# Kernel tuning notes

Measured on AMD Instinct MI355X. Metric: run time of the kernel, lower is better.

Reference implementation:

```python
import jax, jax.numpy as jnp
import numpy as np

N_NODES = 100000


def _sage_conv(x, edge_index, W_n, W_s, b):
    # edge_index: [2, E] with row0 = src, row1 = dst (messages flow src -> dst)
    src, dst = edge_index[0], edge_index[1]
    msgs = x[src]                                   # [E, F] gather
    summed = jax.ops.segment_sum(msgs, dst, num_segments=N_NODES)   # [N, F]
    deg = jax.ops.segment_sum(jnp.ones((edge_index.shape[1],), x.dtype), dst,
                              num_segments=N_NODES)                 # [N]
    mean = summed / jnp.maximum(deg, 1.0)[:, None]  # mean aggregation
    return mean @ W_n + x @ W_s + b


def setup_inputs() -> dict:
    key = jax.random.key(0)
    ks = jax.random.split(key, 8)
    in_dim, hid_dim, out_dim = 64, 64, 32
    n_edges = 1600000
    x = jax.random.normal(ks[0], (N_NODES, in_dim), dtype=jnp.float32)
    edge_index = jax.random.randint(ks[1], (2, n_edges), 0, N_NODES, dtype=jnp.int64)
    s1 = 1.0 / np.sqrt(in_dim)
    s2 = 1.0 / np.sqrt(hid_dim)
    W1_n = jax.random.uniform(ks[2], (in_dim, hid_dim), jnp.float32, -s1, s1)
    W1_s = jax.random.uniform(ks[3], (in_dim, hid_dim), jnp.float32, -s1, s1)
    b1 = jnp.zeros((hid_dim,), jnp.float32)
    W2_n = jax.random.uniform(ks[4], (hid_dim, out_dim), jnp.float32, -s2, s2)
    W2_s = jax.random.uniform(ks[5], (hid_dim, out_dim), jnp.float32, -s2, s2)
    b2 = jnp.zeros((out_dim,), jnp.float32)
    return {"x": x, "edge_index": edge_index, "W1_n": W1_n, "W1_s": W1_s,
            "b1": b1, "W2_n": W2_n, "W2_s": W2_s, "b2": b2}


def reference(x, edge_index, W1_n, W1_s, b1, W2_n, W2_s, b2):
    h = _sage_conv(x, edge_index, W1_n, W1_s, b1)
    h = jax.nn.relu(h)
    # dropout(p=0.5) is identity in eval mode
    out = _sage_conv(h, edge_index, W2_n, W2_s, b2)
    return out
```

## Files before the change

kernel.cpp:

```cpp
#include <hip/hip_runtime.h>
#include <hip/hip_bf16.h>

#define N_NODES 100000
#define NB 784
#define NPAD 100352
#define BSH 7
#define BMASK 127
#define CAP 4096

typedef float v2f __attribute__((ext_vector_type(2)));

__device__ inline void fma4(float a, const float4& w, float4& c) {
  c.x = fmaf(a, w.x, c.x);
  c.y = fmaf(a, w.y, c.y);
  c.z = fmaf(a, w.z, c.z);
  c.w = fmaf(a, w.w, c.w);
}
__device__ inline unsigned short f2bf(float f) {
  unsigned u = __float_as_uint(f);
  u += 0x7fffu + ((u >> 16) & 1u);
  return (unsigned short)(u >> 16);
}
__device__ inline unsigned pack2bf(float a, float b) {
  return (unsigned)f2bf(a) | ((unsigned)f2bf(b) << 16);
}
__device__ inline float bf2f(unsigned short u) {
  return __uint_as_float((unsigned)u << 16);
}
__device__ inline unsigned packfp8x4(float a, float b, float c, float d) {
  int pk = __builtin_amdgcn_cvt_pk_fp8_f32(a, b, 0, false);
  pk = __builtin_amdgcn_cvt_pk_fp8_f32(c, d, pk, true);
  return (unsigned)pk;
}
__device__ inline float4 relu_mix(uint2 m, uint2 s) {
  float4 v;
  v.x = fmaxf(__uint_as_float(m.x << 16) + __uint_as_float(s.x << 16), 0.f);
  v.y = fmaxf(__uint_as_float(m.x & 0xffff0000u) +
                  __uint_as_float(s.x & 0xffff0000u), 0.f);
  v.z = fmaxf(__uint_as_float(m.y << 16) + __uint_as_float(s.y << 16), 0.f);
  v.w = fmaxf(__uint_as_float(m.y & 0xffff0000u) +
                  __uint_as_float(s.y & 0xffff0000u), 0.f);
  return v;
}

#define EPB 4096
#define GB1 1563

__global__ __launch_bounds__(256) void fusedA_k(
    const int* __restrict__ src, const int* __restrict__ dst,
    unsigned* __restrict__ bcur, unsigned* __restrict__ ep,
    const float* __restrict__ x, const float* __restrict__ W1n,
    const float* __restrict__ W1s, const float* __restrict__ b1,
    unsigned* __restrict__ xnb8, unsigned short* __restrict__ xsb,
    int E, int NSB, int M) {
  __shared__ __align__(16) float smem[8192];
  const int tid = threadIdx.x;

  if ((int)blockIdx.x < NSB) {
    unsigned* lh = (unsigned*)smem;
    unsigned* lbase = lh + NB;
    for (int i = tid; i < NB; i += 256) lh[i] = 0;
    __syncthreads();
    const int base = blockIdx.x * EPB;
    unsigned short rank[16];
    unsigned short bb[16];
#pragma unroll
    for (int it = 0; it < 16; ++it) {
      int e = base + it * 256 + tid;
      if (e < E) {
        unsigned b = ((unsigned)dst[e]) >> BSH;
        bb[it] = (unsigned short)b;
        rank[it] = (unsigned short)atomicAdd(&lh[b], 1u);
      }
    }
    __syncthreads();
    for (int i = tid; i < NB; i += 256)
      lbase[i] = lh[i] ? atomicAdd(&bcur[i], lh[i]) : 0u;
    __syncthreads();
#pragma unroll
    for (int it = 0; it < 16; ++it) {
      int e = base + it * 256 + tid;
      if (e < E) {
        unsigned b = bb[it];
        ep[(size_t)b * CAP + lbase[b] + rank[it]] =
            (((unsigned)src[e]) << BSH) | (((unsigned)dst[e]) & BMASK);
      }
    }
    return;
  }

  float* Wn = smem;
  float* Ws = smem + 4096;
  const int row0 = ((int)blockIdx.x - NSB) * 64;

  for (int i = tid; i < 1024; i += 256) {
    ((float4*)Wn)[i] = ((const float4*)W1n)[i];
    ((float4*)Ws)[i] = ((const float4*)W1s)[i];
  }

  const int tx = tid & 15;
  const int ty = tid >> 4;
  const int arow = ty * 4;

  const float* xr[4];
#pragma unroll
  for (int r = 0; r < 4; ++r) {
    long long gr = row0 + arow + r;
    if (gr >= M) gr = M - 1;
    xr[r] = x + gr * 64;
  }

  float4 an[4], as[4];
#pragma unroll
  for (int r = 0; r < 4; ++r) {
    an[r] = make_float4(0.f, 0.f, 0.f, 0.f);
    as[r] = make_float4(0.f, 0.f, 0.f, 0.f);
  }
  __syncthreads();

#pragma unroll 2
  for (int k4 = 0; k4 < 16; ++k4) {
    float4 a[4];
#pragma unroll
    for (int r = 0; r < 4; ++r) a[r] = *(const float4*)(xr[r] + 4 * k4);
    float4 wn0 = *(const float4*)&Wn[(4 * k4 + 0) * 64 + 4 * tx];
    float4 wn1 = *(const float4*)&Wn[(4 * k4 + 1) * 64 + 4 * tx];
    float4 wn2 = *(const float4*)&Wn[(4 * k4 + 2) * 64 + 4 * tx];
    float4 wn3 = *(const float4*)&Wn[(4 * k4 + 3) * 64 + 4 * tx];
    float4 ws0 = *(const float4*)&Ws[(4 * k4 + 0) * 64 + 4 * tx];
    float4 ws1 = *(const float4*)&Ws[(4 * k4 + 1) * 64 + 4 * tx];
    float4 ws2 = *(const float4*)&Ws[(4 * k4 + 2) * 64 + 4 * tx];
    float4 ws3 = *(const float4*)&Ws[(4 * k4 + 3) * 64 + 4 * tx];
#pragma unroll
    for (int r = 0; r < 4; ++r) {
      fma4(a[r].x, wn0, an[r]);
      fma4(a[r].y, wn1, an[r]);
      fma4(a[r].z, wn2, an[r]);
      fma4(a[r].w, wn3, an[r]);
      fma4(a[r].x, ws0, as[r]);
      fma4(a[r].y, ws1, as[r]);
      fma4(a[r].z, ws2, as[r]);
      fma4(a[r].w, ws3, as[r]);
    }
  }

  const float4 bv = *(const float4*)&b1[4 * tx];
#pragma unroll
  for (int r = 0; r < 4; ++r) {
    int row = row0 + arow + r;
    if (row < M) {
      ushort4 ps;
      ps.x = f2bf(as[r].x + bv.x);
      ps.y = f2bf(as[r].y + bv.y);
      ps.z = f2bf(as[r].z + bv.z);
      ps.w = f2bf(as[r].w + bv.w);
      *(ushort4*)&xsb[(long long)row * 64 + 4 * tx] = ps;
      xnb8[(size_t)row * 16 + tx] =
          packfp8x4(an[r].x, an[r].y, an[r].z, an[r].w);
    }
  }
}

__global__ __launch_bounds__(256) void bsort_k(const unsigned* __restrict__ ep,
                                               const unsigned* __restrict__ bcur,
                                               int* __restrict__ ssrc,
                                               uint2* __restrict__ rows2) {
  __shared__ unsigned cnt[128];
  __shared__ unsigned sc[128];
  const int tid = threadIdx.x;
  const int b = blockIdx.x;
  const unsigned cntb = bcur[b];
  const unsigned beg = (unsigned)(b * CAP);
  if (tid < 128) cnt[tid] = 0;
  __syncthreads();
  for (unsigned j = tid; j < cntb; j += 256)
    atomicAdd(&cnt[ep[(size_t)beg + j] & BMASK], 1u);
  __syncthreads();
  unsigned v = (tid < 128) ? cnt[tid] : 0u;
  if (tid < 128) sc[tid] = v;
  __syncthreads();
  for (int off = 1; off < 128; off <<= 1) {
    unsigned t = (tid < 128 && tid >= off) ? sc[tid - off] : 0u;
    __syncthreads();
    if (tid < 128) sc[tid] += t;
    __syncthreads();
  }
  if (tid < 128) {
    unsigned ex = sc[tid] - v;
    rows2[b * 128 + tid] = make_uint2(beg + ex, beg + ex + v);
    cnt[tid] = ex;
  }
  __syncthreads();
  for (unsigned j = tid; j < cntb; j += 256) {
    unsigned p = ep[(size_t)beg + j];
    unsigned r = atomicAdd(&cnt[p & BMASK], 1u);
    ssrc[(size_t)beg + r] = (int)(p >> BSH);
  }
}

#define MSTRIDE 36

__global__ __launch_bounds__(256) void fgg_k(
    const uint4* __restrict__ valb4, const int* __restrict__ ssrc,
    const uint2* __restrict__ rows2, const unsigned short* __restrict__ xsb,
    const float* __restrict__ W2n, const float* __restrict__ W2s,
    const float* __restrict__ b2, unsigned* __restrict__ hnb8,
    float* __restrict__ hs, int M) {
  __shared__ float Wn[64 * 32];
  __shared__ float Ws[64 * 32];
  __shared__ unsigned mlds[64 * MSTRIDE];
  const int tid = threadIdx.x;
  const int node0 = blockIdx.x * 64;

  for (int i = tid; i < 512; i += 256) {
    ((float4*)Wn)[i] = ((const float4*)W2n)[i];
    ((float4*)Ws)[i] = ((const float4*)W2s)[i];
  }

  constexpr int P = 4;
  const int lrow = tid / P;
  const int node = node0 + lrow;
  const int p = tid & 3;
  const uint2 be = rows2[node];
  const unsigned beg = be.x, end = be.y;

  float acc[16];
#pragma unroll
  for (int q = 0; q < 16; ++q) acc[q] = 0.f;

  unsigned j = beg;
  for (; j + 8 <= end; j += 8) {
    int sn[8];
#pragma unroll
    for (int i = 0; i < 8; ++i) sn[i] = ssrc[j + i];
    uint4 u[8];
#pragma unroll
    for (int i = 0; i < 8; ++i) u[i] = valb4[(size_t)sn[i] * P + p];
#pragma unroll
    for (int i = 0; i < 8; ++i) {
      v2f f0 = __builtin_amdgcn_cvt_pk_f32_fp8((int)u[i].x, false);
      v2f f1 = __builtin_amdgcn_cvt_pk_f32_fp8((int)u[i].x, true);
      v2f f2 = __builtin_amdgcn_cvt_pk_f32_fp8((int)u[i].y, false);
      v2f f3 = __builtin_amdgcn_cvt_pk_f32_fp8((int)u[i].y, true);
      v2f f4 = __builtin_amdgcn_cvt_pk_f32_fp8((int)u[i].z, false);
      v2f f5 = __builtin_amdgcn_cvt_pk_f32_fp8((int)u[i].z, true);
      v2f f6 = __builtin_amdgcn_cvt_pk_f32_fp8((int)u[i].w, false);
      v2f f7 = __builtin_amdgcn_cvt_pk_f32_fp8((int)u[i].w, true);
      acc[0] += f0[0];  acc[1] += f0[1];
      acc[2] += f1[0];  acc[3] += f1[1];
      acc[4] += f2[0];  acc[5] += f2[1];
      acc[6] += f3[0];  acc[7] += f3[1];
      acc[8] += f4[0];  acc[9] += f4[1];
      acc[10] += f5[0]; acc[11] += f5[1];
      acc[12] += f6[0]; acc[13] += f6[1];
      acc[14] += f7[0]; acc[15] += f7[1];
    }
  }
  if (j < end) {
    const unsigned last = end - 1;
    int sn[8];
#pragma unroll
    for (int i = 0; i < 8; ++i) {
      unsigned jj = j + i;
      sn[i] = ssrc[jj < last ? jj : last];
    }
    uint4 u[8];
#pragma unroll
    for (int i = 0; i < 8; ++i) u[i] = valb4[(size_t)sn[i] * P + p];
#pragma unroll
    for (int i = 0; i < 8; ++i) {
      float w = ((j + i) < end) ? 1.f : 0.f;
      v2f f0 = __builtin_amdgcn_cvt_pk_f32_fp8((int)u[i].x, false);
      v2f f1 = __builtin_amdgcn_cvt_pk_f32_fp8((int)u[i].x, true);
      v2f f2 = __builtin_amdgcn_cvt_pk_f32_fp8((int)u[i].y, false);
      v2f f3 = __builtin_amdgcn_cvt_pk_f32_fp8((int)u[i].y, true);
      v2f f4 = __builtin_amdgcn_cvt_pk_f32_fp8((int)u[i].z, false);
      v2f f5 = __builtin_amdgcn_cvt_pk_f32_fp8((int)u[i].z, true);
      v2f f6 = __builtin_amdgcn_cvt_pk_f32_fp8((int)u[i].w, false);
      v2f f7 = __builtin_amdgcn_cvt_pk_f32_fp8((int)u[i].w, true);
      acc[0] = fmaf(w, f0[0], acc[0]);   acc[1] = fmaf(w, f0[1], acc[1]);
      acc[2] = fmaf(w, f1[0], acc[2]);   acc[3] = fmaf(w, f1[1], acc[3]);
      acc[4] = fmaf(w, f2[0], acc[4]);   acc[5] = fmaf(w, f2[1], acc[5]);
      acc[6] = fmaf(w, f3[0], acc[6]);   acc[7] = fmaf(w, f3[1], acc[7]);
      acc[8] = fmaf(w, f4[0], acc[8]);   acc[9] = fmaf(w, f4[1], acc[9]);
      acc[10] = fmaf(w, f5[0], acc[10]); acc[11] = fmaf(w, f5[1], acc[11]);
      acc[12] = fmaf(w, f6[0], acc[12]); acc[13] = fmaf(w, f6[1], acc[13]);
      acc[14] = fmaf(w, f7[0], acc[14]); acc[15] = fmaf(w, f7[1], acc[15]);
    }
  }

  const unsigned dg = end - beg;
  const float inv = dg ? 1.f / (float)dg : 0.f;
  uint4 pk0, pk1;
  pk0.x = pack2bf(acc[0] * inv, acc[1] * inv);
  pk0.y = pack2bf(acc[2] * inv, acc[3] * inv);
  pk0.z = pack2bf(acc[4] * inv, acc[5] * inv);
  pk0.w = pack2bf(acc[6] * inv, acc[7] * inv);
  pk1.x = pack2bf(acc[8] * inv, acc[9] * inv);
  pk1.y = pack2bf(acc[10] * inv, acc[11] * inv);
  pk1.z = pack2bf(acc[12] * inv, acc[13] * inv);
  pk1.w = pack2bf(acc[14] * inv, acc[15] * inv);
  *(uint4*)&mlds[lrow * MSTRIDE + p * 8] = pk0;
  *(uint4*)&mlds[lrow * MSTRIDE + p * 8 + 4] = pk1;
  __syncthreads();

  const int tx = tid & 7;
  const int ty = tid >> 3;
  const int arow = ty * 2;

  const uint2* mp[2];
  const uint2* sp[2];
#pragma unroll
  for (int r = 0; r < 2; ++r) {
    long long gr = node0 + arow + r;
    if (gr >= M) gr = M - 1;
    mp[r] = (const uint2*)&mlds[(arow + r) * MSTRIDE];
    sp[r] = (const uint2*)(xsb + gr * 64);
  }

  float4 an[2], as[2];
#pragma unroll
  for (int r = 0; r < 2; ++r) {
    an[r] = make_float4(0.f, 0.f, 0.f, 0.f);
    as[r] = make_float4(0.f, 0.f, 0.f, 0.f);
  }

#pragma unroll 2
  for (int k4 = 0; k4 < 16; ++k4) {
    float4 a[2];
#pragma unroll
    for (int r = 0; r < 2; ++r) a[r] = relu_mix(mp[r][k4], sp[r][k4]);
    float4 wn0 = *(const float4*)&Wn[(4 * k4 + 0) * 32 + 4 * tx];
    float4 wn1 = *(const float4*)&Wn[(4 * k4 + 1) * 32 + 4 * tx];
    float4 wn2 = *(const float4*)&Wn[(4 * k4 + 2) * 32 + 4 * tx];
    float4 wn3 = *(const float4*)&Wn[(4 * k4 + 3) * 32 + 4 * tx];
    float4 ws0 = *(const float4*)&Ws[(4 * k4 + 0) * 32 + 4 * tx];
    float4 ws1 = *(const float4*)&Ws[(4 * k4 + 1) * 32 + 4 * tx];
    float4 ws2 = *(const float4*)&Ws[(4 * k4 + 2) * 32 + 4 * tx];
    float4 ws3 = *(const float4*)&Ws[(4 * k4 + 3) * 32 + 4 * tx];
#pragma unroll
    for (int r = 0; r < 2; ++r) {
      fma4(a[r].x, wn0, an[r]);
      fma4(a[r].y, wn1, an[r]);
      fma4(a[r].z, wn2, an[r]);
      fma4(a[r].w, wn3, an[r]);
      fma4(a[r].x, ws0, as[r]);
      fma4(a[r].y, ws1, as[r]);
      fma4(a[r].z, ws2, as[r]);
      fma4(a[r].w, ws3, as[r]);
    }
  }

  const float4 bv = *(const float4*)&b2[4 * tx];
#pragma unroll
  for (int r = 0; r < 2; ++r) {
    int row = node0 + arow + r;
    if (row < M) {
      float4 o;
      o.x = as[r].x + bv.x;
      o.y = as[r].y + bv.y;
      o.z = as[r].z + bv.z;
      o.w = as[r].w + bv.w;
      *(float4*)&hs[(long long)row * 32 + 4 * tx] = o;
      hnb8[(size_t)row * 8 + tx] =
          packfp8x4(an[r].x, an[r].y, an[r].z, an[r].w);
    }
  }
}

__global__ __launch_bounds__(256) void gather2_k(
    const uint4* __restrict__ valb4, const int* __restrict__ ssrc,
    const uint2* __restrict__ rows2, const float* __restrict__ base,
    float* __restrict__ out, int N) {
  constexpr int P = 2;
  const int node = blockIdx.x * 128 + threadIdx.x / P;
  const int p = threadIdx.x & 1;
  if (node >= N) return;
  const uint2 be = rows2[node];
  const unsigned beg = be.x, end = be.y;

  float acc[16];
#pragma unroll
  for (int q = 0; q < 16; ++q) acc[q] = 0.f;

  unsigned j = beg;
  for (; j + 8 <= end; j += 8) {
    int sn[8];
#pragma unroll
    for (int i = 0; i < 8; ++i) sn[i] = ssrc[j + i];
    uint4 u[8];
#pragma unroll
    for (int i = 0; i < 8; ++i) u[i] = valb4[(size_t)sn[i] * P + p];
#pragma unroll
    for (int i = 0; i < 8; ++i) {
      v2f f0 = __builtin_amdgcn_cvt_pk_f32_fp8((int)u[i].x, false);
      v2f f1 = __builtin_amdgcn_cvt_pk_f32_fp8((int)u[i].x, true);
      v2f f2 = __builtin_amdgcn_cvt_pk_f32_fp8((int)u[i].y, false);
      v2f f3 = __builtin_amdgcn_cvt_pk_f32_fp8((int)u[i].y, true);
      v2f f4 = __builtin_amdgcn_cvt_pk_f32_fp8((int)u[i].z, false);
      v2f f5 = __builtin_amdgcn_cvt_pk_f32_fp8((int)u[i].z, true);
      v2f f6 = __builtin_amdgcn_cvt_pk_f32_fp8((int)u[i].w, false);
      v2f f7 = __builtin_amdgcn_cvt_pk_f32_fp8((int)u[i].w, true);
      acc[0] += f0[0];  acc[1] += f0[1];
      acc[2] += f1[0];  acc[3] += f1[1];
      acc[4] += f2[0];  acc[5] += f2[1];
      acc[6] += f3[0];  acc[7] += f3[1];
      acc[8] += f4[0];  acc[9] += f4[1];
      acc[10] += f5[0]; acc[11] += f5[1];
      acc[12] += f6[0]; acc[13] += f6[1];
      acc[14] += f7[0]; acc[15] += f7[1];
    }
  }
  if (j < end) {
    const unsigned last = end - 1;
    int sn[8];
#pragma unroll
    for (int i = 0; i < 8; ++i) {
      unsigned jj = j + i;
      sn[i] = ssrc[jj < last ? jj : last];
    }
    uint4 u[8];
#pragma unroll
    for (int i = 0; i < 8; ++i) u[i] = valb4[(size_t)sn[i] * P + p];
#pragma unroll
    for (int i = 0; i < 8; ++i) {
      float w = ((j + i) < end) ? 1.f : 0.f;
      v2f f0 = __builtin_amdgcn_cvt_pk_f32_fp8((int)u[i].x, false);
      v2f f1 = __builtin_amdgcn_cvt_pk_f32_fp8((int)u[i].x, true);
      v2f f2 = __builtin_amdgcn_cvt_pk_f32_fp8((int)u[i].y, false);
      v2f f3 = __builtin_amdgcn_cvt_pk_f32_fp8((int)u[i].y, true);
      v2f f4 = __builtin_amdgcn_cvt_pk_f32_fp8((int)u[i].z, false);
      v2f f5 = __builtin_amdgcn_cvt_pk_f32_fp8((int)u[i].z, true);
      v2f f6 = __builtin_amdgcn_cvt_pk_f32_fp8((int)u[i].w, false);
      v2f f7 = __builtin_amdgcn_cvt_pk_f32_fp8((int)u[i].w, true);
      acc[0] = fmaf(w, f0[0], acc[0]);   acc[1] = fmaf(w, f0[1], acc[1]);
      acc[2] = fmaf(w, f1[0], acc[2]);   acc[3] = fmaf(w, f1[1], acc[3]);
      acc[4] = fmaf(w, f2[0], acc[4]);   acc[5] = fmaf(w, f2[1], acc[5]);
      acc[6] = fmaf(w, f3[0], acc[6]);   acc[7] = fmaf(w, f3[1], acc[7]);
      acc[8] = fmaf(w, f4[0], acc[8]);   acc[9] = fmaf(w, f4[1], acc[9]);
      acc[10] = fmaf(w, f5[0], acc[10]); acc[11] = fmaf(w, f5[1], acc[11]);
      acc[12] = fmaf(w, f6[0], acc[12]); acc[13] = fmaf(w, f6[1], acc[13]);
      acc[14] = fmaf(w, f7[0], acc[14]); acc[15] = fmaf(w, f7[1], acc[15]);
    }
  }

  const unsigned dg = end - beg;
  const float inv = dg ? 1.f / (float)dg : 0.f;
  const size_t o = (size_t)node * 32 + 16 * p;
#pragma unroll
  for (int q4 = 0; q4 < 4; ++q4) {
    float4 bv = *(const float4*)&base[o + 4 * q4];
    float4 ov;
    ov.x = acc[4 * q4 + 0] * inv + bv.x;
    ov.y = acc[4 * q4 + 1] * inv + bv.y;
    ov.z = acc[4 * q4 + 2] * inv + bv.z;
    ov.w = acc[4 * q4 + 3] * inv + bv.w;
    *(float4*)&out[o + 4 * q4] = ov;
  }
}

extern "C" void kernel_launch(void* const* d_in, const int* in_sizes, int n_in,
                              void* d_out, int out_size, void* d_ws,
                              size_t ws_size, hipStream_t stream) {
  const float* x   = (const float*)d_in[0];
  const int*   ei  = (const int*)d_in[1];
  const float* W1n = (const float*)d_in[2];
  const float* W1s = (const float*)d_in[3];
  const float* b1  = (const float*)d_in[4];
  const float* W2n = (const float*)d_in[5];
  const float* W2s = (const float*)d_in[6];
  const float* b2  = (const float*)d_in[7];
  float* out = (float*)d_out;

  const int E = in_sizes[1] / 2;
  const int M = N_NODES;
  const int* src = ei;
  const int* dst = ei + E;
  const int NSB = (E + EPB - 1) / EPB;

  char* wsb = (char*)d_ws;
  unsigned*       ep    = (unsigned*)(wsb);
  int*            ssrc  = (int*)(wsb + 12845056);
  uint2*          rows2 = (uint2*)(wsb + 25690112);
  unsigned*       bcur  = (unsigned*)(wsb + 26492928);
  unsigned*       xnb8  = (unsigned*)(wsb + 26496064);
  unsigned short* xsb   = (unsigned short*)(wsb + 32896064);
  float*          hs    = (float*)(wsb + 45696064);
  unsigned*       hnb8  = (unsigned*)(wsb);

  hipMemsetAsync(bcur, 0, NB * 4, stream);
  fusedA_k<<<NSB + GB1, 256, 0, stream>>>(src, dst, bcur, ep, x, W1n, W1s, b1,
                                          xnb8, xsb, E, NSB, M);
  bsort_k<<<NB, 256, 0, stream>>>(ep, bcur, ssrc, rows2);
  fgg_k<<<GB1, 256, 0, stream>>>((const uint4*)xnb8, ssrc, rows2, xsb, W2n,
                                 W2s, b2, hnb8, hs, M);
  gather2_k<<<(M + 127) / 128, 256, 0, stream>>>((const uint4*)hnb8, ssrc,
                                                 rows2, hs, out, M);
}
```

Measured before the change: 198.8 us.

## Fuse edge bucketing into layer-1 GEMM and bucket sort into layer-1 gather

Every layer-1 GEMM block now loads the weights, and the first NSB of them also scatter a 2048-edge chunk into dst buckets before doing their GEMM tile. The separate bucket-sort kernel is merged into the first gather+GEMM kernel: each block sorts one 128-node bucket, keeps the sorted source ids in LDS when they fit, and then aggregates and multiplies two 64-node halves. The intent is to remove a kernel launch and its round trip through global memory, and to reuse the sorted indices from LDS. In exchange the fused kernel runs fewer, heavier blocks (784 instead of 1563) and uses more LDS, which may lower occupancy. hnb8 is moved to its own workspace region because it can no longer alias ep.

```diff
diff --git a/kernel.cpp b/kernel.cpp
--- a/kernel.cpp
+++ b/kernel.cpp
@@ -7,6 +7,8 @@
 #define BSH 7
 #define BMASK 127
 #define CAP 4096
+#define LCAP 3584
+#define MSTRIDE 36
 
 typedef float v2f __attribute__((ext_vector_type(2)));
 
@@ -23,9 +25,6 @@
 }
 __device__ inline unsigned pack2bf(float a, float b) {
   return (unsigned)f2bf(a) | ((unsigned)f2bf(b) << 16);
-}
-__device__ inline float bf2f(unsigned short u) {
-  return __uint_as_float((unsigned)u << 16);
 }
 __device__ inline unsigned packfp8x4(float a, float b, float c, float d) {
   int pk = __builtin_amdgcn_cvt_pk_fp8_f32(a, b, 0, false);
@@ -43,10 +42,11 @@
   return v;
 }
 
-#define EPB 4096
+#define EPB 2048
+#define EPT 8
 #define GB1 1563
 
-__global__ __launch_bounds__(256) void fusedA_k(
+__global__ __launch_bounds__(256, 5) void fusedA_k(
     const int* __restrict__ src, const int* __restrict__ dst,
     unsigned* __restrict__ bcur, unsigned* __restrict__ ep,
     const float* __restrict__ x, const float* __restrict__ W1n,
@@ -54,23 +54,32 @@
     unsigned* __restrict__ xnb8, unsigned short* __restrict__ xsb,
     int E, int NSB, int M) {
   __shared__ __align__(16) float smem[8192];
+  float* Wn = smem;
+  float* Ws = smem + 4096;
+  unsigned* lh = (unsigned*)Ws;
+  unsigned* lbase = lh + NB;
   const int tid = threadIdx.x;
-
-  if ((int)blockIdx.x < NSB) {
-    unsigned* lh = (unsigned*)smem;
-    unsigned* lbase = lh + NB;
+  const int bid = blockIdx.x;
+
+  for (int i = tid; i < 1024; i += 256)
+    ((float4*)Wn)[i] = ((const float4*)W1n)[i];
+
+  if (bid < NSB) {
     for (int i = tid; i < NB; i += 256) lh[i] = 0;
     __syncthreads();
-    const int base = blockIdx.x * EPB;
-    unsigned short rank[16];
-    unsigned short bb[16];
-#pragma unroll
-    for (int it = 0; it < 16; ++it) {
-      int e = base + it * 256 + tid;
+    const int ebase = bid * EPB;
+    int es[EPT], ed[EPT];
+    unsigned short rk[EPT], bb[EPT];
+#pragma unroll
+    for (int it = 0; it < EPT; ++it) {
+      int e = ebase + it * 256 + tid;
       if (e < E) {
-        unsigned b = ((unsigned)dst[e]) >> BSH;
-        bb[it] = (unsigned short)b;
-        rank[it] = (unsigned short)atomicAdd(&lh[b], 1u);
+        int d = dst[e];
+        es[it] = src[e];
+        ed[it] = d;
+        unsigned bkt = ((unsigned)d) >> BSH;
+        bb[it] = (unsigned short)bkt;
+        rk[it] = (unsigned short)atomicAdd(&lh[bkt], 1u);
       }
     }
     __syncthreads();
@@ -78,26 +87,21 @@
       lbase[i] = lh[i] ? atomicAdd(&bcur[i], lh[i]) : 0u;
     __syncthreads();
 #pragma unroll
-    for (int it = 0; it < 16; ++it) {
-      int e = base + it * 256 + tid;
+    for (int it = 0; it < EPT; ++it) {
+      int e = ebase + it * 256 + tid;
       if (e < E) {
-        unsigned b = bb[it];
-        ep[(size_t)b * CAP + lbase[b] + rank[it]] =
-            (((unsigned)src[e]) << BSH) | (((unsigned)dst[e]) & BMASK);
-      }
-    }
-    return;
-  }
-
-  float* Wn = smem;
-  float* Ws = smem + 4096;
-  const int row0 = ((int)blockIdx.x - NSB) * 64;
-
-  for (int i = tid; i < 1024; i += 256) {
-    ((float4*)Wn)[i] = ((const float4*)W1n)[i];
+        unsigned bkt = bb[it];
+        ep[(size_t)bkt * CAP + lbase[bkt] + rk[it]] =
+            (((unsigned)es[it]) << BSH) | (((unsigned)ed[it]) & BMASK);
+      }
+    }
+    __syncthreads();
+  }
+
+  for (int i = tid; i < 1024; i += 256)
     ((float4*)Ws)[i] = ((const float4*)W1s)[i];
-  }
-
+
+  const int row0 = bid * 64;
   const int tx = tid & 15;
   const int ty = tid >> 4;
   const int arow = ty * 4;
@@ -161,18 +165,31 @@
   }
 }
 
-__global__ __launch_bounds__(256) void bsort_k(const unsigned* __restrict__ ep,
-                                               const unsigned* __restrict__ bcur,
-                                               int* __restrict__ ssrc,
-                                               uint2* __restrict__ rows2) {
+__global__ __launch_bounds__(256, 4) void fggs_k(
+    const uint4* __restrict__ valb4, const unsigned* __restrict__ ep,
+    const unsigned* __restrict__ bcur, int* __restrict__ ssrc,
+    uint2* __restrict__ rows2, const unsigned short* __restrict__ xsb,
+    const float* __restrict__ W2n, const float* __restrict__ W2s,
+    const float* __restrict__ b2, unsigned* __restrict__ hnb8,
+    float* __restrict__ hs, int M) {
+  __shared__ float Wn[64 * 32];
+  __shared__ float Ws[64 * 32];
+  __shared__ unsigned ssrc_l[LCAP];
+  __shared__ unsigned mlds[64 * MSTRIDE];
   __shared__ unsigned cnt[128];
   __shared__ unsigned sc[128];
   const int tid = threadIdx.x;
   const int b = blockIdx.x;
   const unsigned cntb = bcur[b];
   const unsigned beg = (unsigned)(b * CAP);
+
+  for (int i = tid; i < 512; i += 256) {
+    ((float4*)Wn)[i] = ((const float4*)W2n)[i];
+    ((float4*)Ws)[i] = ((const float4*)W2s)[i];
+  }
   if (tid < 128) cnt[tid] = 0;
   __syncthreads();
+
   for (unsigned j = tid; j < cntb; j += 256)
     atomicAdd(&cnt[ep[(size_t)beg + j] & BMASK], 1u);
   __syncthreads();
@@ -188,39 +205,188 @@
   if (tid < 128) {
     unsigned ex = sc[tid] - v;
     rows2[b * 128 + tid] = make_uint2(beg + ex, beg + ex + v);
-    cnt[tid] = ex;
-  }
+    cnt[tid] = ex | (v << 16);
+  }
+  __syncthreads();
+  const int ln = tid >> 2;
+  const int p4 = tid & 3;
+  const unsigned cpk0 = cnt[ln];
+  const unsigned cpk1 = cnt[64 + ln];
   __syncthreads();
   for (unsigned j = tid; j < cntb; j += 256) {
-    unsigned p = ep[(size_t)beg + j];
-    unsigned r = atomicAdd(&cnt[p & BMASK], 1u);
-    ssrc[(size_t)beg + r] = (int)(p >> BSH);
-  }
-}
-
-#define MSTRIDE 36
-
-__global__ __launch_bounds__(256) void fgg_k(
+    unsigned pv = ep[(size_t)beg + j];
+    unsigned r = atomicAdd(&cnt[pv & BMASK], 1u) & 0xffffu;
+    unsigned s = pv >> BSH;
+    ssrc[(size_t)beg + r] = (int)s;
+    if (r < LCAP) ssrc_l[r] = s;
+  }
+  __syncthreads();
+
+  const unsigned* sl = (cntb <= (unsigned)LCAP)
+                           ? (const unsigned*)ssrc_l
+                           : (const unsigned*)ssrc + beg;
+
+#pragma unroll
+  for (int pp = 0; pp < 2; ++pp) {
+    const unsigned cpk = pp ? cpk1 : cpk0;
+    const unsigned lbeg = cpk & 0xffffu;
+    const unsigned dg = cpk >> 16;
+    const unsigned lend = lbeg + dg;
+
+    float acc[16];
+#pragma unroll
+    for (int q = 0; q < 16; ++q) acc[q] = 0.f;
+
+    unsigned j = lbeg;
+    for (; j + 8 <= lend; j += 8) {
+      unsigned sn[8];
+#pragma unroll
+      for (int i = 0; i < 8; ++i) sn[i] = sl[j + i];
+      uint4 u[8];
+#pragma unroll
+      for (int i = 0; i < 8; ++i) u[i] = valb4[(size_t)sn[i] * 4 + p4];
+#pragma unroll
+      for (int i = 0; i < 8; ++i) {
+        v2f f0 = __builtin_amdgcn_cvt_pk_f32_fp8((int)u[i].x, false);
+        v2f f1 = __builtin_amdgcn_cvt_pk_f32_fp8((int)u[i].x, true);
+        v2f f2 = __builtin_amdgcn_cvt_pk_f32_fp8((int)u[i].y, false);
+        v2f f3 = __builtin_amdgcn_cvt_pk_f32_fp8((int)u[i].y, true);
+        v2f f4 = __builtin_amdgcn_cvt_pk_f32_fp8((int)u[i].z, false);
+        v2f f5 = __builtin_amdgcn_cvt_pk_f32_fp8((int)u[i].z, true);
+        v2f f6 = __builtin_amdgcn_cvt_pk_f32_fp8((int)u[i].w, false);
+        v2f f7 = __builtin_amdgcn_cvt_pk_f32_fp8((int)u[i].w, true);
+        acc[0] += f0[0];  acc[1] += f0[1];
+        acc[2] += f1[0];  acc[3] += f1[1];
+        acc[4] += f2[0];  acc[5] += f2[1];
+        acc[6] += f3[0];  acc[7] += f3[1];
+        acc[8] += f4[0];  acc[9] += f4[1];
+        acc[10] += f5[0]; acc[11] += f5[1];
+        acc[12] += f6[0]; acc[13] += f6[1];
+        acc[14] += f7[0]; acc[15] += f7[1];
+      }
+    }
+    if (j < lend) {
+      const unsigned last = lend - 1;
+      unsigned sn[8];
+#pragma unroll
+      for (int i = 0; i < 8; ++i) {
+        unsigned jj = j + i;
+        sn[i] = sl[jj < last ? jj : last];
+      }
+      uint4 u[8];
+#pragma unroll
+      for (int i = 0; i < 8; ++i) u[i] = valb4[(size_t)sn[i] * 4 + p4];
+#pragma unroll
+      for (int i = 0; i < 8; ++i) {
+        float w = ((j + i) < lend) ? 1.f : 0.f;
+        v2f f0 = __builtin_amdgcn_cvt_pk_f32_fp8((int)u[i].x, false);
+        v2f f1 = __builtin_amdgcn_cvt_pk_f32_fp8((int)u[i].x, true);
+        v2f f2 = __builtin_amdgcn_cvt_pk_f32_fp8((int)u[i].y, false);
+        v2f f3 = __builtin_amdgcn_cvt_pk_f32_fp8((int)u[i].y, true);
+        v2f f4 = __builtin_amdgcn_cvt_pk_f32_fp8((int)u[i].z, false);
+        v2f f5 = __builtin_amdgcn_cvt_pk_f32_fp8((int)u[i].z, true);
+        v2f f6 = __builtin_amdgcn_cvt_pk_f32_fp8((int)u[i].w, false);
+        v2f f7 = __builtin_amdgcn_cvt_pk_f32_fp8((int)u[i].w, true);
+        acc[0] = fmaf(w, f0[0], acc[0]);   acc[1] = fmaf(w, f0[1], acc[1]);
+        acc[2] = fmaf(w, f1[0], acc[2]);   acc[3] = fmaf(w, f1[1], acc[3]);
+        acc[4] = fmaf(w, f2[0], acc[4]);   acc[5] = fmaf(w, f2[1], acc[5]);
+        acc[6] = fmaf(w, f3[0], acc[6]);   acc[7] = fmaf(w, f3[1], acc[7]);
+        acc[8] = fmaf(w, f4[0], acc[8]);   acc[9] = fmaf(w, f4[1], acc[9]);
+        acc[10] = fmaf(w, f5[0], acc[10]); acc[11] = fmaf(w, f5[1], acc[11]);
+        acc[12] = fmaf(w, f6[0], acc[12]); acc[13] = fmaf(w, f6[1], acc[13]);
+        acc[14] = fmaf(w, f7[0], acc[14]); acc[15] = fmaf(w, f7[1], acc[15]);
+      }
+    }
+
+    const float inv = dg ? 1.f / (float)dg : 0.f;
+    uint4 pk0, pk1;
+    pk0.x = pack2bf(acc[0] * inv, acc[1] * inv);
+    pk0.y = pack2bf(acc[2] * inv, acc[3] * inv);
+    pk0.z = pack2bf(acc[4] * inv, acc[5] * inv);
+    pk0.w = pack2bf(acc[6] * inv, acc[7] * inv);
+    pk1.x = pack2bf(acc[8] * inv, acc[9] * inv);
+    pk1.y = pack2bf(acc[10] * inv, acc[11] * inv);
+    pk1.z = pack2bf(acc[12] * inv, acc[13] * inv);
+    pk1.w = pack2bf(acc[14] * inv, acc[15] * inv);
+    *(uint4*)&mlds[ln * MSTRIDE + p4 * 8] = pk0;
+    *(uint4*)&mlds[ln * MSTRIDE + p4 * 8 + 4] = pk1;
+    __syncthreads();
+
+    const int tx = tid & 7;
+    const int ty = tid >> 3;
+    const int arow = ty * 2;
+    const int node0p = b * 128 + pp * 64;
+
+    const uint2* mp[2];
+    const uint2* sp[2];
+#pragma unroll
+    for (int r = 0; r < 2; ++r) {
+      long long gr = node0p + arow + r;
+      if (gr >= M) gr = M - 1;
+      mp[r] = (const uint2*)&mlds[(arow + r) * MSTRIDE];
+      sp[r] = (const uint2*)(xsb + gr * 64);
+    }
+
+    float4 an[2], as[2];
+#pragma unroll
+    for (int r = 0; r < 2; ++r) {
+      an[r] = make_float4(0.f, 0.f, 0.f, 0.f);
+      as[r] = make_float4(0.f, 0.f, 0.f, 0.f);
+    }
+
+#pragma unroll 2
+    for (int k4 = 0; k4 < 16; ++k4) {
+      float4 a[2];
+#pragma unroll
+      for (int r = 0; r < 2; ++r) a[r] = relu_mix(mp[r][k4], sp[r][k4]);
+      float4 wn0 = *(const float4*)&Wn[(4 * k4 + 0) * 32 + 4 * tx];
+      float4 wn1 = *(const float4*)&Wn[(4 * k4 + 1) * 32 + 4 * tx];
+      float4 wn2 = *(const float4*)&Wn[(4 * k4 + 2) * 32 + 4 * tx];
+      float4 wn3 = *(const float4*)&Wn[(4 * k4 + 3) * 32 + 4 * tx];
+      float4 ws0 = *(const float4*)&Ws[(4 * k4 + 0) * 32 + 4 * tx];
+      float4 ws1 = *(const float4*)&Ws[(4 * k4 + 1) * 32 + 4 * tx];
+      float4 ws2 = *(const float4*)&Ws[(4 * k4 + 2) * 32 + 4 * tx];
+      float4 ws3 = *(const float4*)&Ws[(4 * k4 + 3) * 32 + 4 * tx];
+#pragma unroll
+      for (int r = 0; r < 2; ++r) {
+        fma4(a[r].x, wn0, an[r]);
+        fma4(a[r].y, wn1, an[r]);
+        fma4(a[r].z, wn2, an[r]);
+        fma4(a[r].w, wn3, an[r]);
+        fma4(a[r].x, ws0, as[r]);
+        fma4(a[r].y, ws1, as[r]);
+        fma4(a[r].z, ws2, as[r]);
+        fma4(a[r].w, ws3, as[r]);
+      }
+    }
+
+    const float4 bvv = *(const float4*)&b2[4 * tx];
+#pragma unroll
+    for (int r = 0; r < 2; ++r) {
+      int row = node0p + arow + r;
+      if (row < M) {
+        float4 o;
+        o.x = as[r].x + bvv.x;
+        o.y = as[r].y + bvv.y;
+        o.z = as[r].z + bvv.z;
+        o.w = as[r].w + bvv.w;
+        *(float4*)&hs[(long long)row * 32 + 4 * tx] = o;
+        hnb8[(size_t)row * 8 + tx] =
+            packfp8x4(an[r].x, an[r].y, an[r].z, an[r].w);
+      }
+    }
+    __syncthreads();
+  }
+}
+
+__global__ __launch_bounds__(256) void gather2_k(
     const uint4* __restrict__ valb4, const int* __restrict__ ssrc,
-    const uint2* __restrict__ rows2, const unsigned short* __restrict__ xsb,
-    const float* __restrict__ W2n, const float* __restrict__ W2s,
-    const float* __restrict__ b2, unsigned* __restrict__ hnb8,
-    float* __restrict__ hs, int M) {
-  __shared__ float Wn[64 * 32];
-  __shared__ float Ws[64 * 32];
-  __shared__ unsigned mlds[64 * MSTRIDE];
-  const int tid = threadIdx.x;
-  const int node0 = blockIdx.x * 64;
-
-  for (int i = tid; i < 512; i += 256) {
-    ((float4*)Wn)[i] = ((const float4*)W2n)[i];
-    ((float4*)Ws)[i] = ((const float4*)W2s)[i];
-  }
-
-  constexpr int P = 4;
-  const int lrow = tid / P;
-  const int node = node0 + lrow;
-  const int p = tid & 3;
+    const uint2* __restrict__ rows2, const float* __restrict__ base,
+    float* __restrict__ out, int N) {
+  constexpr int P = 2;
+  const int node = blockIdx.x * 128 + threadIdx.x / P;
+  const int p = threadIdx.x & 1;
+  if (node >= N) return;
   const uint2 be = rows2[node];
   const unsigned beg = be.x, end = be.y;
 
@@ -291,161 +457,6 @@
 
   const unsigned dg = end - beg;
   const float inv = dg ? 1.f / (float)dg : 0.f;
-  uint4 pk0, pk1;
-  pk0.x = pack2bf(acc[0] * inv, acc[1] * inv);
-  pk0.y = pack2bf(acc[2] * inv, acc[3] * inv);
-  pk0.z = pack2bf(acc[4] * inv, acc[5] * inv);
-  pk0.w = pack2bf(acc[6] * inv, acc[7] * inv);
-  pk1.x = pack2bf(acc[8] * inv, acc[9] * inv);
-  pk1.y = pack2bf(acc[10] * inv, acc[11] * inv);
-  pk1.z = pack2bf(acc[12] * inv, acc[13] * inv);
-  pk1.w = pack2bf(acc[14] * inv, acc[15] * inv);
-  *(uint4*)&mlds[lrow * MSTRIDE + p * 8] = pk0;
-  *(uint4*)&mlds[lrow * MSTRIDE + p * 8 + 4] = pk1;
-  __syncthreads();
-
-  const int tx = tid & 7;
-  const int ty = tid >> 3;
-  const int arow = ty * 2;
-
-  const uint2* mp[2];
-  const uint2* sp[2];
-#pragma unroll
-  for (int r = 0; r < 2; ++r) {
-    long long gr = node0 + arow + r;
-    if (gr >= M) gr = M - 1;
-    mp[r] = (const uint2*)&mlds[(arow + r) * MSTRIDE];
-    sp[r] = (const uint2*)(xsb + gr * 64);
-  }
-
-  float4 an[2], as[2];
-#pragma unroll
-  for (int r = 0; r < 2; ++r) {
-    an[r] = make_float4(0.f, 0.f, 0.f, 0.f);
-    as[r] = make_float4(0.f, 0.f, 0.f, 0.f);
-  }
-
-#pragma unroll 2
-  for (int k4 = 0; k4 < 16; ++k4) {
-    float4 a[2];
-#pragma unroll
-    for (int r = 0; r < 2; ++r) a[r] = relu_mix(mp[r][k4], sp[r][k4]);
-    float4 wn0 = *(const float4*)&Wn[(4 * k4 + 0) * 32 + 4 * tx];
-    float4 wn1 = *(const float4*)&Wn[(4 * k4 + 1) * 32 + 4 * tx];
-    float4 wn2 = *(const float4*)&Wn[(4 * k4 + 2) * 32 + 4 * tx];
-    float4 wn3 = *(const float4*)&Wn[(4 * k4 + 3) * 32 + 4 * tx];
-    float4 ws0 = *(const float4*)&Ws[(4 * k4 + 0) * 32 + 4 * tx];
-    float4 ws1 = *(const float4*)&Ws[(4 * k4 + 1) * 32 + 4 * tx];
-    float4 ws2 = *(const float4*)&Ws[(4 * k4 + 2) * 32 + 4 * tx];
-    float4 ws3 = *(const float4*)&Ws[(4 * k4 + 3) * 32 + 4 * tx];
-#pragma unroll
-    for (int r = 0; r < 2; ++r) {
-      fma4(a[r].x, wn0, an[r]);
-      fma4(a[r].y, wn1, an[r]);
-      fma4(a[r].z, wn2, an[r]);
-      fma4(a[r].w, wn3, an[r]);
-      fma4(a[r].x, ws0, as[r]);
-      fma4(a[r].y, ws1, as[r]);
-      fma4(a[r].z, ws2, as[r]);
-      fma4(a[r].w, ws3, as[r]);
-    }
-  }
-
-  const float4 bv = *(const float4*)&b2[4 * tx];
-#pragma unroll
-  for (int r = 0; r < 2; ++r) {
-    int row = node0 + arow + r;
-    if (row < M) {
-      float4 o;
-      o.x = as[r].x + bv.x;
-      o.y = as[r].y + bv.y;
-      o.z = as[r].z + bv.z;
-      o.w = as[r].w + bv.w;
-      *(float4*)&hs[(long long)row * 32 + 4 * tx] = o;
-      hnb8[(size_t)row * 8 + tx] =
-          packfp8x4(an[r].x, an[r].y, an[r].z, an[r].w);
-    }
-  }
-}
-
-__global__ __launch_bounds__(256) void gather2_k(
-    const uint4* __restrict__ valb4, const int* __restrict__ ssrc,
-    const uint2* __restrict__ rows2, const float* __restrict__ base,
-    float* __restrict__ out, int N) {
-  constexpr int P = 2;
-  const int node = blockIdx.x * 128 + threadIdx.x / P;
-  const int p = threadIdx.x & 1;
-  if (node >= N) return;
-  const uint2 be = rows2[node];
-  const unsigned beg = be.x, end = be.y;
-
-  float acc[16];
-#pragma unroll
-  for (int q = 0; q < 16; ++q) acc[q] = 0.f;
-
-  unsigned j = beg;
-  for (; j + 8 <= end; j += 8) {
-    int sn[8];
-#pragma unroll
-    for (int i = 0; i < 8; ++i) sn[i] = ssrc[j + i];
-    uint4 u[8];
-#pragma unroll
-    for (int i = 0; i < 8; ++i) u[i] = valb4[(size_t)sn[i] * P + p];
-#pragma unroll
-    for (int i = 0; i < 8; ++i) {
-      v2f f0 = __builtin_amdgcn_cvt_pk_f32_fp8((int)u[i].x, false);
-      v2f f1 = __builtin_amdgcn_cvt_pk_f32_fp8((int)u[i].x, true);
-      v2f f2 = __builtin_amdgcn_cvt_pk_f32_fp8((int)u[i].y, false);
-      v2f f3 = __builtin_amdgcn_cvt_pk_f32_fp8((int)u[i].y, true);
-      v2f f4 = __builtin_amdgcn_cvt_pk_f32_fp8((int)u[i].z, false);
-      v2f f5 = __builtin_amdgcn_cvt_pk_f32_fp8((int)u[i].z, true);
-      v2f f6 = __builtin_amdgcn_cvt_pk_f32_fp8((int)u[i].w, false);
-      v2f f7 = __builtin_amdgcn_cvt_pk_f32_fp8((int)u[i].w, true);
-      acc[0] += f0[0];  acc[1] += f0[1];
-      acc[2] += f1[0];  acc[3] += f1[1];
-      acc[4] += f2[0];  acc[5] += f2[1];
-      acc[6] += f3[0];  acc[7] += f3[1];
-      acc[8] += f4[0];  acc[9] += f4[1];
-      acc[10] += f5[0]; acc[11] += f5[1];
-      acc[12] += f6[0]; acc[13] += f6[1];
-      acc[14] += f7[0]; acc[15] += f7[1];
-    }
-  }
-  if (j < end) {
-    const unsigned last = end - 1;
-    int sn[8];
-#pragma unroll
-    for (int i = 0; i < 8; ++i) {
-      unsigned jj = j + i;
-      sn[i] = ssrc[jj < last ? jj : last];
-    }
-    uint4 u[8];
-#pragma unroll
-    for (int i = 0; i < 8; ++i) u[i] = valb4[(size_t)sn[i] * P + p];
-#pragma unroll
-    for (int i = 0; i < 8; ++i) {
-      float w = ((j + i) < end) ? 1.f : 0.f;
-      v2f f0 = __builtin_amdgcn_cvt_pk_f32_fp8((int)u[i].x, false);
-      v2f f1 = __builtin_amdgcn_cvt_pk_f32_fp8((int)u[i].x, true);
-      v2f f2 = __builtin_amdgcn_cvt_pk_f32_fp8((int)u[i].y, false);
-      v2f f3 = __builtin_amdgcn_cvt_pk_f32_fp8((int)u[i].y, true);
-      v2f f4 = __builtin_amdgcn_cvt_pk_f32_fp8((int)u[i].z, false);
-      v2f f5 = __builtin_amdgcn_cvt_pk_f32_fp8((int)u[i].z, true);
-      v2f f6 = __builtin_amdgcn_cvt_pk_f32_fp8((int)u[i].w, false);
-      v2f f7 = __builtin_amdgcn_cvt_pk_f32_fp8((int)u[i].w, true);
-      acc[0] = fmaf(w, f0[0], acc[0]);   acc[1] = fmaf(w, f0[1], acc[1]);
-      acc[2] = fmaf(w, f1[0], acc[2]);   acc[3] = fmaf(w, f1[1], acc[3]);
-      acc[4] = fmaf(w, f2[0], acc[4]);   acc[5] = fmaf(w, f2[1], acc[5]);
-      acc[6] = fmaf(w, f3[0], acc[6]);   acc[7] = fmaf(w, f3[1], acc[7]);
-      acc[8] = fmaf(w, f4[0], acc[8]);   acc[9] = fmaf(w, f4[1], acc[9]);
-      acc[10] = fmaf(w, f5[0], acc[10]); acc[11] = fmaf(w, f5[1], acc[11]);
-      acc[12] = fmaf(w, f6[0], acc[12]); acc[13] = fmaf(w, f6[1], acc[13]);
-      acc[14] = fmaf(w, f7[0], acc[14]); acc[15] = fmaf(w, f7[1], acc[15]);
-    }
-  }
-
-  const unsigned dg = end - beg;
-  const float inv = dg ? 1.f / (float)dg : 0.f;
   const size_t o = (size_t)node * 32 + 16 * p;
 #pragma unroll
   for (int q4 = 0; q4 < 4; ++q4) {
@@ -485,15 +496,14 @@
   unsigned*       bcur  = (unsigned*)(wsb + 26492928);
   unsigned*       xnb8  = (unsigned*)(wsb + 26496064);
   unsigned short* xsb   = (unsigned short*)(wsb + 32896064);
-  float*          hs    = (float*)(wsb + 45696064);
-  unsigned*       hnb8  = (unsigned*)(wsb);
+  unsigned*       hnb8  = (unsigned*)(wsb + 45696064);
+  float*          hs    = (float*)(wsb + 58496064);
 
   hipMemsetAsync(bcur, 0, NB * 4, stream);
-  fusedA_k<<<NSB + GB1, 256, 0, stream>>>(src, dst, bcur, ep, x, W1n, W1s, b1,
-                                          xnb8, xsb, E, NSB, M);
-  bsort_k<<<NB, 256, 0, stream>>>(ep, bcur, ssrc, rows2);
-  fgg_k<<<GB1, 256, 0, stream>>>((const uint4*)xnb8, ssrc, rows2, xsb, W2n,
-                                 W2s, b2, hnb8, hs, M);
+  fusedA_k<<<GB1, 256, 0, stream>>>(src, dst, bcur, ep, x, W1n, W1s, b1,
+                                    xnb8, xsb, E, NSB, M);
+  fggs_k<<<NB, 256, 0, stream>>>((const uint4*)xnb8, ep, bcur, ssrc, rows2,
+                                 xsb, W2n, W2s, b2, hnb8, hs, M);
   gather2_k<<<(M + 127) / 128, 256, 0, stream>>>((const uint4*)hnb8, ssrc,
                                                  rows2, hs, out, M);
 }
```

Result: slower. 251.0 us (+26.3%).
